# Kernel optimization log

Measured on AMD Instinct MI355X. Metric: run time of the kernel, lower is better.

Reference implementation:

```python
import jax, jax.numpy as jnp
import numpy as np

N_LAYERS = 3
D = 32          # in = hidden = out channels (hardcoded in module)
N = 100_000     # nodes
E = 3_200_000   # edges (avg degree 32)
EPS = 1e-5
SLOPE = 0.01    # LeakyReLU default negative slope


def setup_inputs() -> dict:
    key = jax.random.key(0)
    ks = jax.random.split(key, 12)
    x = jax.random.normal(ks[0], (N, D), jnp.float32)
    edge_index = jax.random.randint(ks[1], (2, E), 0, N)
    edge_attr = jax.random.normal(ks[2], (E, 1), jnp.float32)  # unused by the conv
    s = 1.0 / np.sqrt(D)  # torch Linear default init range
    W = lambda k: jax.random.uniform(k, (N_LAYERS, D, D), jnp.float32, -s, s)
    b = lambda k: jax.random.uniform(k, (N_LAYERS, D), jnp.float32, -s, s)
    return dict(
        patch_embs=x, edge_index=edge_index, edge_attr=edge_attr,
        Wk=W(ks[3]), bk=b(ks[4]),   # lin_key   (applied to x_i / target)
        Wq=W(ks[5]), bq=b(ks[6]),   # lin_query (applied to x_j / source)
        Wv=W(ks[7]), bv=b(ks[8]),   # lin_value (applied to x_j / source)
        Ws=W(ks[9]), bs=b(ks[10]),  # lin_skip  (applied to x_i)
        gamma=jnp.ones((N_LAYERS, D), jnp.float32),
        beta=jnp.zeros((N_LAYERS, D), jnp.float32),
    )


def _res_gated_conv(x, Wk, bk, Wq, bq, Wv, bv, Ws, bs, src, dst):
    # Project per-node first (cheap), gather per-edge after.
    k = x @ Wk.T + bk   # [N,D] key   of target
    q = x @ Wq.T + bq   # [N,D] query of source
    v = x @ Wv.T + bv   # [N,D] value of source
    eta = jax.nn.sigmoid(k[dst] + q[src])          # [E,D] gate
    agg = jax.ops.segment_sum(eta * v[src], dst, num_segments=x.shape[0])
    return agg + (x @ Ws.T + bs)


def _batchnorm(x, g, b):
    mu = x.mean(axis=0)
    var = x.var(axis=0)  # biased, as in torch BN training forward
    return (x - mu) * jax.lax.rsqrt(var + EPS) * g + b


def _leaky(z):
    return jnp.where(z >= 0, z, SLOPE * z)


def reference(patch_embs, edge_index, edge_attr, Wk, bk, Wq, bq, Wv, bv, Ws, bs, gamma, beta):
    src, dst = edge_index[0], edge_index[1]
    h = patch_embs
    h = _batchnorm(_leaky(_res_gated_conv(h, Wk[0], bk[0], Wq[0], bq[0], Wv[0], bv[0], Ws[0], bs[0], src, dst)) + h, gamma[0], beta[0])
    h = _batchnorm(_leaky(_res_gated_conv(h, Wk[1], bk[1], Wq[1], bq[1], Wv[1], bv[1], Ws[1], bs[1], src, dst)) + h, gamma[1], beta[1])
    h = _batchnorm(_res_gated_conv(h, Wk[2], bk[2], Wq[2], bq[2], Wv[2], bv[2], Ws[2], bs[2], src, dst) + h, gamma[2], beta[2])
    return h
```

## Files before the change

kernel.cpp:

```cpp
#include <hip/hip_runtime.h>

#define DCH 32
#define EPSV 1e-5f
#define SLOPE 0.01f
#define SSTRIDE 16
#define BSH 7
#define BSZ 128
#define NBMAX 1024
#define CHUNK 8192
#define CAP 6144
#define LOG2E 1.4426950408889634f

#if defined(__has_builtin)
#  if __has_builtin(__builtin_amdgcn_exp2f)
#    define EXP2F(x) __builtin_amdgcn_exp2f(x)
#  endif
#  if __has_builtin(__builtin_amdgcn_rcpf)
#    define RCPF(x) __builtin_amdgcn_rcpf(x)
#  endif
#endif
#ifndef EXP2F
#  define EXP2F(x) exp2f(x)
#endif
#ifndef RCPF
#  define RCPF(x) (1.0f / (x))
#endif

__device__ __forceinline__ unsigned short f2bf(float x) {
    unsigned u = __float_as_uint(x);
    unsigned r = (u + 0x7FFFu + ((u >> 16) & 1u)) >> 16;
    return (unsigned short)r;
}

__global__ __launch_bounds__(256) void k_bucket_hist(const int* __restrict__ dst,
                                                     int* __restrict__ bcnt, int E, int NB) {
    __shared__ int h[NBMAX];
    const int t = threadIdx.x;
    const int e0 = blockIdx.x * CHUNK;
    const int e1 = min(e0 + CHUNK, E);
    if (NB <= NBMAX) {
        for (int j = t; j < NB; j += 256) h[j] = 0;
        __syncthreads();
        for (int e = e0 + t; e < e1; e += 256) atomicAdd(&h[dst[e] >> BSH], 1);
        __syncthreads();
        for (int j = t; j < NB; j += 256) if (h[j]) atomicAdd(&bcnt[j], h[j]);
    } else {
        for (int e = e0 + t; e < e1; e += 256) atomicAdd(&bcnt[dst[e] >> BSH], 1);
    }
}

__global__ __launch_bounds__(1024) void k_scan(const int* __restrict__ deg, int* __restrict__ off, int N) {
    __shared__ int wsum[16];
    __shared__ int woff[16];
    __shared__ int ctot;
    __shared__ int carry;
    const int t = threadIdx.x;
    const int lane = t & 63;
    const int w = t >> 6;
    if (t == 0) carry = 0;
    __syncthreads();
    for (int base = 0; base < N; base += 1024) {
        const int i = base + t;
        const int v = (i < N) ? deg[i] : 0;
        int incl = v;
        #pragma unroll
        for (int d = 1; d < 64; d <<= 1) {
            int tmp = __shfl_up(incl, d);
            if (lane >= d) incl += tmp;
        }
        if (lane == 63) wsum[w] = incl;
        __syncthreads();
        if (t < 16) {
            const int a = wsum[t];
            int in = a;
            #pragma unroll
            for (int d = 1; d < 16; d <<= 1) {
                int tmp = __shfl_up(in, d);
                if (t >= d) in += tmp;
            }
            woff[t] = in - a;
            if (t == 15) ctot = in;
        }
        __syncthreads();
        if (i < N) off[i] = carry + woff[w] + incl - v;
        __syncthreads();
        if (t == 0) carry += ctot;
        __syncthreads();
    }
    if (t == 0) off[N] = carry;
}

__global__ __launch_bounds__(256) void k_bucket_scatter(const int* __restrict__ src, const int* __restrict__ dst,
                                                        const int* __restrict__ boff, int* __restrict__ cur,
                                                        unsigned int* __restrict__ pairs, int E, int NB) {
    const int t = threadIdx.x;
    const int e0 = blockIdx.x * CHUNK;
    const int e1 = min(e0 + CHUNK, E);
    if (NB <= NBMAX) {
        __shared__ int cnt[NBMAX];
        __shared__ int base[NBMAX];
        for (int j = t; j < NB; j += 256) { cnt[j] = 0; }
        __syncthreads();
        for (int e = e0 + t; e < e1; e += 256) atomicAdd(&cnt[dst[e] >> BSH], 1);
        __syncthreads();
        for (int j = t; j < NB; j += 256) {
            const int c = cnt[j];
            if (c) base[j] = atomicAdd(&cur[j], c);
            cnt[j] = 0;
        }
        __syncthreads();
        for (int e = e0 + t; e < e1; e += 256) {
            const int d = dst[e];
            const int bk = d >> BSH;
            const int r = atomicAdd(&cnt[bk], 1);
            pairs[boff[bk] + base[bk] + r] = ((unsigned)src[e] << BSH) | (unsigned)(d & (BSZ - 1));
        }
    } else {
        for (int e = e0 + t; e < e1; e += 256) {
            const int d = dst[e];
            const int bk = d >> BSH;
            const int r = atomicAdd(&cur[bk], 1);
            pairs[boff[bk] + r] = ((unsigned)src[e] << BSH) | (unsigned)(d & (BSZ - 1));
        }
    }
}

__global__ __launch_bounds__(256) void k_build_csr(const unsigned int* __restrict__ pairs,
                                                   const int* __restrict__ boff,
                                                   int* __restrict__ deg, int* __restrict__ off,
                                                   int* __restrict__ ssrc, int N) {
    __shared__ int cnt[BSZ];
    __shared__ int scn[BSZ];
    __shared__ int rnk[BSZ];
    __shared__ int stage[CAP];
    const int t = threadIdx.x;
    const int b = blockIdx.x;
    const int begin = boff[b], end = boff[b + 1];
    const int total = end - begin;
    if (t < BSZ) { cnt[t] = 0; rnk[t] = 0; }
    __syncthreads();
    for (int i = begin + t; i < end; i += 256) atomicAdd(&cnt[pairs[i] & (BSZ - 1)], 1);
    __syncthreads();
    if (t < BSZ) scn[t] = cnt[t];
    __syncthreads();
    #pragma unroll
    for (int s = 1; s < BSZ; s <<= 1) {
        int add = 0;
        if (t < BSZ && t >= s) add = scn[t - s];
        __syncthreads();
        if (t < BSZ) scn[t] += add;
        __syncthreads();
    }
    const int node0 = b << BSH;
    if (t < BSZ && node0 + t < N) {
        deg[node0 + t] = cnt[t];
        off[node0 + t] = begin + scn[t] - cnt[t];
    }
    if (total <= CAP) {
        for (int i = begin + t; i < end; i += 256) {
            const unsigned u = pairs[i];
            const int nl = u & (BSZ - 1);
            const int r = atomicAdd(&rnk[nl], 1);
            stage[scn[nl] - cnt[nl] + r] = (int)(u >> BSH);
        }
        __syncthreads();
        for (int i = t; i < total; i += 256) ssrc[begin + i] = stage[i];
    } else {
        for (int i = begin + t; i < end; i += 256) {
            const unsigned u = pairs[i];
            const int nl = u & (BSZ - 1);
            const int r = atomicAdd(&rnk[nl], 1);
            ssrc[begin + scn[nl] - cnt[nl] + r] = (int)(u >> BSH);
        }
    }
}

__global__ __launch_bounds__(256) void k_project(
    const float* __restrict__ xin,
    const float* __restrict__ statsPrev, const float* __restrict__ gPrev, const float* __restrict__ bPrev,
    const float* __restrict__ Wk, const float* __restrict__ bk,
    const float* __restrict__ Wq, const float* __restrict__ bq,
    const float* __restrict__ Wv, const float* __restrict__ bv,
    const float* __restrict__ Ws, const float* __restrict__ bs,
    float* __restrict__ kout, uint4* __restrict__ qvout,
    float* __restrict__ zout, float* __restrict__ statsCur,
    int N, int do_bn, float invN)
{
    __shared__ float wk[DCH][DCH + 1], wq[DCH][DCH + 1], wv[DCH][DCH + 1], wsk[DCH][DCH + 1];
    __shared__ float xs[8][DCH];
    __shared__ unsigned short qvs[8][64];
    const int t = threadIdx.x;
    if (blockIdx.x == 0) {
        for (int i = t; i < 2048; i += 256) statsCur[i] = 0.f;
    }
    for (int i = t; i < DCH * DCH; i += 256) {
        const int c = i >> 5, d = i & 31;
        wk[c][d] = Wk[i];
        wq[c][d] = Wq[i];
        wv[c][d] = Wv[i];
        wsk[c][d] = Ws[i];
    }
    const int li = t >> 5;
    const int c  = t & 31;
    const int node = blockIdx.x * 8 + li;
    if (node < N) {
        float xv = xin[node * DCH + c];
        if (do_bn) {
            const float mn = statsPrev[c * SSTRIDE] * invN;
            const float var = statsPrev[1024 + c * SSTRIDE] * invN - mn * mn;
            const float sc = rsqrtf(var + EPSV) * gPrev[c];
            xv = (xv - mn) * sc + bPrev[c];
        }
        xs[li][c] = xv;
    }
    __syncthreads();
    if (node < N) {
        float aK = 0.f, aQ = 0.f, aV = 0.f, aS = 0.f;
        #pragma unroll
        for (int d = 0; d < DCH; ++d) {
            const float xv = xs[li][d];
            aK += xv * wk[c][d];
            aQ += xv * wq[c][d];
            aV += xv * wv[c][d];
            aS += xv * wsk[c][d];
        }
        const int o = node * DCH + c;
        kout[o] = -LOG2E * (aK + bk[c]);
        zout[o] = aS + bs[c];
        const int g = c >> 2, j = c & 3;
        qvs[li][g * 8 + j]     = f2bf(-LOG2E * (aQ + bq[c]));
        qvs[li][g * 8 + 4 + j] = f2bf(aV + bv[c]);
    }
    __syncthreads();
    if (t < 64) {
        const int ln = t >> 3, g = t & 7;
        const int nd = blockIdx.x * 8 + ln;
        if (nd < N) qvout[nd * 8 + g] = ((const uint4*)qvs[ln])[g];
    }
}

#define GATE_ACC(u, ax, ay, az, aw)                                          \
    do {                                                                     \
        const float q0 = __uint_as_float((u).x << 16);                       \
        const float q1 = __uint_as_float((u).x & 0xffff0000u);               \
        const float q2 = __uint_as_float((u).y << 16);                       \
        const float q3 = __uint_as_float((u).y & 0xffff0000u);               \
        const float v0 = __uint_as_float((u).z << 16);                       \
        const float v1 = __uint_as_float((u).z & 0xffff0000u);               \
        const float v2 = __uint_as_float((u).w << 16);                       \
        const float v3 = __uint_as_float((u).w & 0xffff0000u);               \
        ax = fmaf(v0, RCPF(1.f + EXP2F(kn.x + q0)), ax);                     \
        ay = fmaf(v1, RCPF(1.f + EXP2F(kn.y + q1)), ay);                     \
        az = fmaf(v2, RCPF(1.f + EXP2F(kn.z + q2)), az);                     \
        aw = fmaf(v3, RCPF(1.f + EXP2F(kn.w + q3)), aw);                     \
    } while (0)

__global__ __launch_bounds__(256) void k_edges_csr(
    const int* __restrict__ off, const int* __restrict__ deg, const int* __restrict__ ssrc,
    const float4* __restrict__ kn4, const uint4* __restrict__ qv4,
    const float4* __restrict__ zprev4,
    const float* __restrict__ statsPrev, const float* __restrict__ gPrev, const float* __restrict__ bPrev,
    float4* __restrict__ z4,
    float* __restrict__ statsCur, int N, int do_leaky, int do_bn, float invN)
{
    const int t = threadIdx.x;
    const int p = t & 7;
    const int lane = t & 63;
    const int w = t >> 6;
    float scv[4] = {1.f, 1.f, 1.f, 1.f}, shv[4] = {0.f, 0.f, 0.f, 0.f};
    if (do_bn) {
        #pragma unroll
        for (int j = 0; j < 4; ++j) {
            const int c = p * 4 + j;
            const float mn = statsPrev[c * SSTRIDE] * invN;
            const float var = statsPrev[1024 + c * SSTRIDE] * invN - mn * mn;
            const float rs = rsqrtf(var + EPSV) * gPrev[c];
            scv[j] = rs;
            shv[j] = bPrev[c] - mn * rs;
        }
    }
    float s0 = 0.f, s1 = 0.f, s2 = 0.f, s3 = 0.f;
    float r0 = 0.f, r1 = 0.f, r2 = 0.f, r3 = 0.f;
    const int n = blockIdx.x * 32 + (t >> 3);
    if (n < N) {
        const int idx = n * 8 + p;
        const float4 kn = kn4[idx];
        float ax = 0.f, ay = 0.f, az = 0.f, aw = 0.f;
        float bx = 0.f, by = 0.f, bz = 0.f, bw = 0.f;
        const int beg = off[n];
        const int end = beg + deg[n];
        int e = beg;
        for (; e + 4 <= end; e += 4) {
            const int sA = ssrc[e];
            const int sB = ssrc[e + 1];
            const int sC = ssrc[e + 2];
            const int sD = ssrc[e + 3];
            const uint4 uA = qv4[(size_t)sA * 8 + p];
            const uint4 uB = qv4[(size_t)sB * 8 + p];
            const uint4 uC = qv4[(size_t)sC * 8 + p];
            const uint4 uD = qv4[(size_t)sD * 8 + p];
            GATE_ACC(uA, ax, ay, az, aw);
            GATE_ACC(uB, bx, by, bz, bw);
            GATE_ACC(uC, ax, ay, az, aw);
            GATE_ACC(uD, bx, by, bz, bw);
        }
        for (; e < end; ++e) {
            const int s = ssrc[e];
            const uint4 u = qv4[(size_t)s * 8 + p];
            GATE_ACC(u, ax, ay, az, aw);
        }
        ax += bx; ay += by; az += bz; aw += bw;
        float4 z = z4[idx];
        z.x += ax; z.y += ay; z.z += az; z.w += aw;
        if (do_leaky) {
            z.x = z.x >= 0.f ? z.x : SLOPE * z.x;
            z.y = z.y >= 0.f ? z.y : SLOPE * z.y;
            z.z = z.z >= 0.f ? z.z : SLOPE * z.z;
            z.w = z.w >= 0.f ? z.w : SLOPE * z.w;
        }
        const float4 hz = zprev4[idx];
        z.x += hz.x * scv[0] + shv[0];
        z.y += hz.y * scv[1] + shv[1];
        z.z += hz.z * scv[2] + shv[2];
        z.w += hz.w * scv[3] + shv[3];
        z4[idx] = z;
        s0 = z.x; s1 = z.y; s2 = z.z; s3 = z.w;
        r0 = z.x * z.x; r1 = z.y * z.y; r2 = z.z * z.z; r3 = z.w * z.w;
    }
    #pragma unroll
    for (int d = 8; d < 64; d <<= 1) {
        s0 += __shfl_down(s0, d); s1 += __shfl_down(s1, d);
        s2 += __shfl_down(s2, d); s3 += __shfl_down(s3, d);
        r0 += __shfl_down(r0, d); r1 += __shfl_down(r1, d);
        r2 += __shfl_down(r2, d); r3 += __shfl_down(r3, d);
    }
    __shared__ float sm[4][DCH], sq[4][DCH];
    if (lane < 8) {
        sm[w][p * 4 + 0] = s0; sm[w][p * 4 + 1] = s1; sm[w][p * 4 + 2] = s2; sm[w][p * 4 + 3] = s3;
        sq[w][p * 4 + 0] = r0; sq[w][p * 4 + 1] = r1; sq[w][p * 4 + 2] = r2; sq[w][p * 4 + 3] = r3;
    }
    __syncthreads();
    if (t < DCH) {
        const float a = sm[0][t] + sm[1][t] + sm[2][t] + sm[3][t];
        const float b = sq[0][t] + sq[1][t] + sq[2][t] + sq[3][t];
        atomicAdd(&statsCur[t * SSTRIDE], a);
        atomicAdd(&statsCur[1024 + t * SSTRIDE], b);
    }
}

__global__ __launch_bounds__(256) void k_bn(
    const float* __restrict__ z, const float* __restrict__ stats,
    const float* __restrict__ gamma, const float* __restrict__ beta,
    float* __restrict__ out, int total, float invN)
{
    const int i = blockIdx.x * 256 + threadIdx.x;
    if (i >= total) return;
    const int c = i & 31;
    const float mean = stats[c * SSTRIDE] * invN;
    const float var  = stats[1024 + c * SSTRIDE] * invN - mean * mean;
    out[i] = (z[i] - mean) * rsqrtf(var + EPSV) * gamma[c] + beta[c];
}

extern "C" void kernel_launch(void* const* d_in, const int* in_sizes, int n_in,
                              void* d_out, int out_size, void* d_ws, size_t ws_size,
                              hipStream_t stream) {
    const float* x     = (const float*)d_in[0];
    const int*   ei    = (const int*)  d_in[1];
    const float* Wk    = (const float*)d_in[3];
    const float* bk    = (const float*)d_in[4];
    const float* Wq    = (const float*)d_in[5];
    const float* bq    = (const float*)d_in[6];
    const float* Wv    = (const float*)d_in[7];
    const float* bv    = (const float*)d_in[8];
    const float* Ws    = (const float*)d_in[9];
    const float* bs    = (const float*)d_in[10];
    const float* gamma = (const float*)d_in[11];
    const float* beta  = (const float*)d_in[12];

    const int N = in_sizes[0] / DCH;
    const int E = in_sizes[1] / 2;
    const int NB = (N + BSZ - 1) >> BSH;
    const int* src = ei;
    const int* dst = ei + E;

    float* ws     = (float*)d_ws;
    float* kbuf   = ws;
    unsigned short* qvbuf = (unsigned short*)(kbuf + (size_t)N * DCH);
    float* zA     = (float*)qvbuf + (size_t)N * DCH;
    float* zB     = zA + (size_t)N * DCH;
    float* statsA = zB + (size_t)N * DCH;
    float* statsB = statsA + 2048;
    int*   deg    = (int*)(statsB + 2048);
    int*   off    = deg + N;
    int*   bcnt   = off + N;
    int*   boff   = bcnt + NB;
    int*   cur    = boff + NB + 1;
    unsigned int* pairs = (unsigned int*)(cur + NB);
    int*   ssrc   = (int*)(pairs + E);

    const int total = N * DCH;
    const float invN = 1.f / (float)N;

    hipMemsetAsync(bcnt, 0, (size_t)NB * sizeof(int), stream);
    hipMemsetAsync(cur, 0, (size_t)NB * sizeof(int), stream);
    const int nchunk = (E + CHUNK - 1) / CHUNK;
    k_bucket_hist<<<nchunk, 256, 0, stream>>>(dst, bcnt, E, NB);
    k_scan<<<1, 1024, 0, stream>>>(bcnt, boff, NB);
    k_bucket_scatter<<<nchunk, 256, 0, stream>>>(src, dst, boff, cur, pairs, E, NB);
    k_build_csr<<<NB, 256, 0, stream>>>(pairs, boff, deg, off, ssrc, N);

    const float* zprev = x;
    const float* statsPrev = nullptr;
    for (int l = 0; l < 3; ++l) {
        const size_t wo = (size_t)l * DCH * DCH;
        const size_t bo = (size_t)l * DCH;
        float* zcur = (l & 1) ? zB : zA;
        float* statsCur = (l & 1) ? statsB : statsA;
        const float* gPrev = (l > 0) ? gamma + (size_t)(l - 1) * DCH : gamma;
        const float* bPrev = (l > 0) ? beta + (size_t)(l - 1) * DCH : beta;
        const int do_bn = (l > 0) ? 1 : 0;
        const float* sPrev = do_bn ? statsPrev : statsA;

        k_project<<<(N + 7) / 8, 256, 0, stream>>>(
            zprev, sPrev, gPrev, bPrev,
            Wk + wo, bk + bo, Wq + wo, bq + bo, Wv + wo, bv + bo, Ws + wo, bs + bo,
            kbuf, (uint4*)qvbuf, zcur, statsCur, N, do_bn, invN);
        k_edges_csr<<<(N + 31) / 32, 256, 0, stream>>>(
            off, deg, ssrc, (const float4*)kbuf, (const uint4*)qvbuf,
            (const float4*)zprev, sPrev, gPrev, bPrev,
            (float4*)zcur, statsCur, N, (l < 2) ? 1 : 0, do_bn, invN);

        statsPrev = statsCur;
        zprev = zcur;
    }
    k_bn<<<(total + 255) / 256, 256, 0, stream>>>(
        zA, statsA, gamma + 2 * DCH, beta + 2 * DCH, (float*)d_out, total, invN);
}
```

Before: 562.1 us.

## Sort CSR neighbor lists by source group for gather locality

Reworks the CSR build so edges are bucketed by (destination block, source group) with 32 source groups, and each node's neighbor list comes out ordered by source range. This is meant to make the per-edge source gathers in the edge kernels more cache-local. The preprocessing now uses global atomics per edge instead of shared-memory aggregated histograms, and runs a single-block scan over a 32x larger count array. Both could make the build more expensive.

Measured after the change: 828.2 us. 1.47x slower.

```diff
diff --git a/kernel.cpp b/kernel.cpp
--- a/kernel.cpp
+++ b/kernel.cpp
@@ -6,9 +6,7 @@
 #define SSTRIDE 16
 #define BSH 7
 #define BSZ 128
-#define NBMAX 1024
-#define CHUNK 8192
-#define CAP 6144
+#define NSG 32
 #define LOG2E 1.4426950408889634f
 
 #if defined(__has_builtin)
@@ -32,21 +30,10 @@
     return (unsigned short)r;
 }
 
-__global__ __launch_bounds__(256) void k_bucket_hist(const int* __restrict__ dst,
-                                                     int* __restrict__ bcnt, int E, int NB) {
-    __shared__ int h[NBMAX];
-    const int t = threadIdx.x;
-    const int e0 = blockIdx.x * CHUNK;
-    const int e1 = min(e0 + CHUNK, E);
-    if (NB <= NBMAX) {
-        for (int j = t; j < NB; j += 256) h[j] = 0;
-        __syncthreads();
-        for (int e = e0 + t; e < e1; e += 256) atomicAdd(&h[dst[e] >> BSH], 1);
-        __syncthreads();
-        for (int j = t; j < NB; j += 256) if (h[j]) atomicAdd(&bcnt[j], h[j]);
-    } else {
-        for (int e = e0 + t; e < e1; e += 256) atomicAdd(&bcnt[dst[e] >> BSH], 1);
-    }
+__global__ __launch_bounds__(256) void k_hist2(const int* __restrict__ src, const int* __restrict__ dst,
+                                               int* __restrict__ cnt, int E, int SGS) {
+    const int e = blockIdx.x * 256 + threadIdx.x;
+    if (e < E) atomicAdd(&cnt[(dst[e] >> BSH) * NSG + (src[e] >> SGS)], 1);
 }
 
 __global__ __launch_bounds__(1024) void k_scan(const int* __restrict__ deg, int* __restrict__ off, int N) {
@@ -90,88 +77,77 @@
     if (t == 0) off[N] = carry;
 }
 
-__global__ __launch_bounds__(256) void k_bucket_scatter(const int* __restrict__ src, const int* __restrict__ dst,
-                                                        const int* __restrict__ boff, int* __restrict__ cur,
-                                                        unsigned int* __restrict__ pairs, int E, int NB) {
-    const int t = threadIdx.x;
-    const int e0 = blockIdx.x * CHUNK;
-    const int e1 = min(e0 + CHUNK, E);
-    if (NB <= NBMAX) {
-        __shared__ int cnt[NBMAX];
-        __shared__ int base[NBMAX];
-        for (int j = t; j < NB; j += 256) { cnt[j] = 0; }
-        __syncthreads();
-        for (int e = e0 + t; e < e1; e += 256) atomicAdd(&cnt[dst[e] >> BSH], 1);
-        __syncthreads();
-        for (int j = t; j < NB; j += 256) {
-            const int c = cnt[j];
-            if (c) base[j] = atomicAdd(&cur[j], c);
-            cnt[j] = 0;
-        }
-        __syncthreads();
-        for (int e = e0 + t; e < e1; e += 256) {
-            const int d = dst[e];
-            const int bk = d >> BSH;
-            const int r = atomicAdd(&cnt[bk], 1);
-            pairs[boff[bk] + base[bk] + r] = ((unsigned)src[e] << BSH) | (unsigned)(d & (BSZ - 1));
-        }
-    } else {
-        for (int e = e0 + t; e < e1; e += 256) {
-            const int d = dst[e];
-            const int bk = d >> BSH;
-            const int r = atomicAdd(&cur[bk], 1);
-            pairs[boff[bk] + r] = ((unsigned)src[e] << BSH) | (unsigned)(d & (BSZ - 1));
-        }
-    }
-}
-
-__global__ __launch_bounds__(256) void k_build_csr(const unsigned int* __restrict__ pairs,
-                                                   const int* __restrict__ boff,
-                                                   int* __restrict__ deg, int* __restrict__ off,
-                                                   int* __restrict__ ssrc, int N) {
-    __shared__ int cnt[BSZ];
-    __shared__ int scn[BSZ];
-    __shared__ int rnk[BSZ];
-    __shared__ int stage[CAP];
+__global__ __launch_bounds__(256) void k_scatter2(const int* __restrict__ src, const int* __restrict__ dst,
+                                                  const int* __restrict__ boff2, int* __restrict__ cur2,
+                                                  unsigned int* __restrict__ pairs, int E, int SGS) {
+    const int e = blockIdx.x * 256 + threadIdx.x;
+    if (e < E) {
+        const int s = src[e];
+        const int d = dst[e];
+        const int key = (d >> BSH) * NSG + (s >> SGS);
+        const int r = atomicAdd(&cur2[key], 1);
+        pairs[boff2[key] + r] = ((unsigned)s << BSH) | (unsigned)(d & (BSZ - 1));
+    }
+}
+
+__global__ __launch_bounds__(256) void k_build_csr2(const unsigned int* __restrict__ pairs,
+                                                    const int* __restrict__ boff2,
+                                                    int* __restrict__ deg, int* __restrict__ off,
+                                                    int* __restrict__ ssrc, int N, int SGS) {
+    __shared__ int cnt2[BSZ * NSG];
+    __shared__ int scn2[BSZ * NSG];
+    __shared__ int rs[BSZ];
+    __shared__ int ex[BSZ];
     const int t = threadIdx.x;
     const int b = blockIdx.x;
-    const int begin = boff[b], end = boff[b + 1];
-    const int total = end - begin;
-    if (t < BSZ) { cnt[t] = 0; rnk[t] = 0; }
-    __syncthreads();
-    for (int i = begin + t; i < end; i += 256) atomicAdd(&cnt[pairs[i] & (BSZ - 1)], 1);
-    __syncthreads();
-    if (t < BSZ) scn[t] = cnt[t];
+    const int begin = boff2[b * NSG];
+    const int end   = boff2[(b + 1) * NSG];
+    for (int i = t; i < BSZ * NSG; i += 256) cnt2[i] = 0;
+    __syncthreads();
+    for (int i = begin + t; i < end; i += 256) {
+        const unsigned u = pairs[i];
+        const int dl = u & (BSZ - 1);
+        const int sg = (u >> BSH) >> SGS;
+        atomicAdd(&cnt2[dl * NSG + sg], 1);
+    }
+    __syncthreads();
+    if (t < BSZ) {
+        int acc = 0;
+        #pragma unroll
+        for (int sg = 0; sg < NSG; ++sg) {
+            scn2[t * NSG + sg] = acc;
+            acc += cnt2[t * NSG + sg];
+        }
+        rs[t] = acc;
+    }
+    __syncthreads();
+    if (t < BSZ) ex[t] = rs[t];
     __syncthreads();
     #pragma unroll
     for (int s = 1; s < BSZ; s <<= 1) {
         int add = 0;
-        if (t < BSZ && t >= s) add = scn[t - s];
-        __syncthreads();
-        if (t < BSZ) scn[t] += add;
+        if (t < BSZ && t >= s) add = ex[t - s];
+        __syncthreads();
+        if (t < BSZ) ex[t] += add;
         __syncthreads();
     }
     const int node0 = b << BSH;
-    if (t < BSZ && node0 + t < N) {
-        deg[node0 + t] = cnt[t];
-        off[node0 + t] = begin + scn[t] - cnt[t];
-    }
-    if (total <= CAP) {
-        for (int i = begin + t; i < end; i += 256) {
-            const unsigned u = pairs[i];
-            const int nl = u & (BSZ - 1);
-            const int r = atomicAdd(&rnk[nl], 1);
-            stage[scn[nl] - cnt[nl] + r] = (int)(u >> BSH);
-        }
-        __syncthreads();
-        for (int i = t; i < total; i += 256) ssrc[begin + i] = stage[i];
-    } else {
-        for (int i = begin + t; i < end; i += 256) {
-            const unsigned u = pairs[i];
-            const int nl = u & (BSZ - 1);
-            const int r = atomicAdd(&rnk[nl], 1);
-            ssrc[begin + scn[nl] - cnt[nl] + r] = (int)(u >> BSH);
-        }
+    if (t < BSZ) {
+        const int base = begin + ex[t] - rs[t];
+        if (node0 + t < N) {
+            deg[node0 + t] = rs[t];
+            off[node0 + t] = base;
+        }
+        #pragma unroll
+        for (int sg = 0; sg < NSG; ++sg) scn2[t * NSG + sg] += base;
+    }
+    __syncthreads();
+    for (int i = begin + t; i < end; i += 256) {
+        const unsigned u = pairs[i];
+        const int dl = u & (BSZ - 1);
+        const int sg = (u >> BSH) >> SGS;
+        const int pos = atomicAdd(&scn2[dl * NSG + sg], 1);
+        ssrc[pos] = (int)(u >> BSH);
     }
 }
 
@@ -380,6 +356,9 @@
     const int N = in_sizes[0] / DCH;
     const int E = in_sizes[1] / 2;
     const int NB = (N + BSZ - 1) >> BSH;
+    const int M  = NB * NSG;
+    int SGS = 0;
+    while (((N - 1) >> SGS) >= NSG) SGS++;
     const int* src = ei;
     const int* dst = ei + E;
 
@@ -392,22 +371,21 @@
     float* statsB = statsA + 2048;
     int*   deg    = (int*)(statsB + 2048);
     int*   off    = deg + N;
-    int*   bcnt   = off + N;
-    int*   boff   = bcnt + NB;
-    int*   cur    = boff + NB + 1;
-    unsigned int* pairs = (unsigned int*)(cur + NB);
+    int*   bcnt2  = off + N;
+    int*   boff2  = bcnt2 + M;
+    int*   cur2   = boff2 + M + 1;
+    unsigned int* pairs = (unsigned int*)(cur2 + M);
     int*   ssrc   = (int*)(pairs + E);
 
     const int total = N * DCH;
     const float invN = 1.f / (float)N;
 
-    hipMemsetAsync(bcnt, 0, (size_t)NB * sizeof(int), stream);
-    hipMemsetAsync(cur, 0, (size_t)NB * sizeof(int), stream);
-    const int nchunk = (E + CHUNK - 1) / CHUNK;
-    k_bucket_hist<<<nchunk, 256, 0, stream>>>(dst, bcnt, E, NB);
-    k_scan<<<1, 1024, 0, stream>>>(bcnt, boff, NB);
-    k_bucket_scatter<<<nchunk, 256, 0, stream>>>(src, dst, boff, cur, pairs, E, NB);
-    k_build_csr<<<NB, 256, 0, stream>>>(pairs, boff, deg, off, ssrc, N);
+    hipMemsetAsync(bcnt2, 0, (size_t)M * sizeof(int), stream);
+    hipMemsetAsync(cur2, 0, (size_t)M * sizeof(int), stream);
+    k_hist2<<<(E + 255) / 256, 256, 0, stream>>>(src, dst, bcnt2, E, SGS);
+    k_scan<<<1, 1024, 0, stream>>>(bcnt2, boff2, M);
+    k_scatter2<<<(E + 255) / 256, 256, 0, stream>>>(src, dst, boff2, cur2, pairs, E, SGS);
+    k_build_csr2<<<NB, 256, 0, stream>>>(pairs, boff2, deg, off, ssrc, N, SGS);
 
     const float* zprev = x;
     const float* statsPrev = nullptr;
```

## Partially sort each node's source list by source-range subgroup in CSR build

Applied to the files above, without the earlier changes.

The CSR build kernel now histograms edges per destination node and per one of 32 coarse source-index ranges, then scatters each source into a slot ordered by that range. Each node's neighbor list ends up roughly sorted by source index, which should give better locality for the per-edge gathers of q and v in the three edge kernels. It drops the shared-memory staging buffer, so the scatter to global memory is less coalesced, and it needs a 128x33 shared counter array.

Result: faster. 550.0 us (-2.2%).

```diff
diff --git a/kernel.cpp b/kernel.cpp
--- a/kernel.cpp
+++ b/kernel.cpp
@@ -8,7 +8,8 @@
 #define BSZ 128
 #define NBMAX 1024
 #define CHUNK 8192
-#define CAP 6144
+#define NSG 32
+#define NSGP 33
 #define LOG2E 1.4426950408889634f
 
 #if defined(__has_builtin)
@@ -125,53 +126,58 @@
     }
 }
 
-__global__ __launch_bounds__(256) void k_build_csr(const unsigned int* __restrict__ pairs,
-                                                   const int* __restrict__ boff,
-                                                   int* __restrict__ deg, int* __restrict__ off,
-                                                   int* __restrict__ ssrc, int N) {
-    __shared__ int cnt[BSZ];
-    __shared__ int scn[BSZ];
-    __shared__ int rnk[BSZ];
-    __shared__ int stage[CAP];
+__global__ __launch_bounds__(256) void k_build_csr2(const unsigned int* __restrict__ pairs,
+                                                    const int* __restrict__ boff,
+                                                    int* __restrict__ deg, int* __restrict__ off,
+                                                    int* __restrict__ ssrc, int N, int SGS) {
+    __shared__ int cnt2[BSZ * NSGP];
+    __shared__ int rs[BSZ];
+    __shared__ int ex[BSZ];
     const int t = threadIdx.x;
     const int b = blockIdx.x;
     const int begin = boff[b], end = boff[b + 1];
-    const int total = end - begin;
-    if (t < BSZ) { cnt[t] = 0; rnk[t] = 0; }
-    __syncthreads();
-    for (int i = begin + t; i < end; i += 256) atomicAdd(&cnt[pairs[i] & (BSZ - 1)], 1);
-    __syncthreads();
-    if (t < BSZ) scn[t] = cnt[t];
+    for (int i = t; i < BSZ * NSGP; i += 256) cnt2[i] = 0;
+    __syncthreads();
+    for (int i = begin + t; i < end; i += 256) {
+        const unsigned u = pairs[i];
+        atomicAdd(&cnt2[(int)(u & (BSZ - 1)) * NSGP + (int)((u >> BSH) >> SGS)], 1);
+    }
+    __syncthreads();
+    if (t < BSZ) {
+        int acc = 0;
+        #pragma unroll
+        for (int sg = 0; sg < NSG; ++sg) {
+            const int c = cnt2[t * NSGP + sg];
+            cnt2[t * NSGP + sg] = acc;
+            acc += c;
+        }
+        rs[t] = acc;
+        ex[t] = acc;
+    }
     __syncthreads();
     #pragma unroll
     for (int s = 1; s < BSZ; s <<= 1) {
         int add = 0;
-        if (t < BSZ && t >= s) add = scn[t - s];
-        __syncthreads();
-        if (t < BSZ) scn[t] += add;
+        if (t < BSZ && t >= s) add = ex[t - s];
+        __syncthreads();
+        if (t < BSZ) ex[t] += add;
         __syncthreads();
     }
     const int node0 = b << BSH;
-    if (t < BSZ && node0 + t < N) {
-        deg[node0 + t] = cnt[t];
-        off[node0 + t] = begin + scn[t] - cnt[t];
-    }
-    if (total <= CAP) {
-        for (int i = begin + t; i < end; i += 256) {
-            const unsigned u = pairs[i];
-            const int nl = u & (BSZ - 1);
-            const int r = atomicAdd(&rnk[nl], 1);
-            stage[scn[nl] - cnt[nl] + r] = (int)(u >> BSH);
-        }
-        __syncthreads();
-        for (int i = t; i < total; i += 256) ssrc[begin + i] = stage[i];
-    } else {
-        for (int i = begin + t; i < end; i += 256) {
-            const unsigned u = pairs[i];
-            const int nl = u & (BSZ - 1);
-            const int r = atomicAdd(&rnk[nl], 1);
-            ssrc[begin + scn[nl] - cnt[nl] + r] = (int)(u >> BSH);
-        }
+    if (t < BSZ) {
+        const int base = begin + ex[t] - rs[t];
+        if (node0 + t < N) {
+            deg[node0 + t] = rs[t];
+            off[node0 + t] = base;
+        }
+        #pragma unroll
+        for (int sg = 0; sg < NSG; ++sg) cnt2[t * NSGP + sg] += base;
+    }
+    __syncthreads();
+    for (int i = begin + t; i < end; i += 256) {
+        const unsigned u = pairs[i];
+        const int pos = atomicAdd(&cnt2[(int)(u & (BSZ - 1)) * NSGP + (int)((u >> BSH) >> SGS)], 1);
+        ssrc[pos] = (int)(u >> BSH);
     }
 }
 
@@ -380,6 +386,8 @@
     const int N = in_sizes[0] / DCH;
     const int E = in_sizes[1] / 2;
     const int NB = (N + BSZ - 1) >> BSH;
+    int SGS = 0;
+    while (((N - 1) >> SGS) >= NSG) SGS++;
     const int* src = ei;
     const int* dst = ei + E;
 
@@ -407,7 +415,7 @@
     k_bucket_hist<<<nchunk, 256, 0, stream>>>(dst, bcnt, E, NB);
     k_scan<<<1, 1024, 0, stream>>>(bcnt, boff, NB);
     k_bucket_scatter<<<nchunk, 256, 0, stream>>>(src, dst, boff, cur, pairs, E, NB);
-    k_build_csr<<<NB, 256, 0, stream>>>(pairs, boff, deg, off, ssrc, N);
+    k_build_csr2<<<NB, 256, 0, stream>>>(pairs, boff, deg, off, ssrc, N, SGS);
 
     const float* zprev = x;
     const float* statsPrev = nullptr;
```
